# Kernel tuning notes

Measured on AMD Instinct MI355X. Metric: run time of the kernel, lower is better.

## Reference

```python
import jax, jax.numpy as jnp
import numpy as np

LEAKY_ALPHA = 0.2
EPS_NORM = 1e-07


def _leaky_relu(x):
    return jnp.where(x >= 0, x, LEAKY_ALPHA * x)


def setup_inputs() -> dict:
    key = jax.random.key(0)
    ks = jax.random.split(key, 10)
    B, N, F = 16, 1024, 256
    H, Q, K, V = 4, 128, 128, 128
    return {
        "e": jax.random.normal(ks[0], (B, N, N), dtype=jnp.float32),
        "x_atm": jax.random.normal(ks[1], (B, N, F), dtype=jnp.float32),
        "mask": jnp.ones((B, N), dtype=jnp.float32),
        "eps": jax.random.normal(ks[2], (1,), dtype=jnp.float32) * 0.02,
        "Wq": jax.random.normal(ks[3], (H, F, Q), dtype=jnp.float32) * 0.05,
        "Wk": jax.random.normal(ks[4], (H, F, K), dtype=jnp.float32) * 0.05,
        "Wv": jax.random.normal(ks[5], (H, F, V), dtype=jnp.float32) * 0.05,
        "aq": jax.random.normal(ks[6], (H, Q), dtype=jnp.float32) * 0.05,
        "bq": jnp.zeros((H,), dtype=jnp.float32),
        "ak": jax.random.normal(ks[7], (H, K), dtype=jnp.float32) * 0.05,
        "bk": jnp.zeros((H,), dtype=jnp.float32),
    }


def reference(e, x_atm, mask, eps, Wq, Wk, Wv, aq, bq, ak, bk):
    B, N, _ = e.shape
    # add learned eps to the diagonal of e (set_diag(diag + eps))
    e_mod = e + eps[0] * jnp.eye(N, dtype=e.dtype)  # [B,N,N]

    # per-head query/key scalars: Dense -> LeakyReLU -> Dense(1)
    q = jnp.einsum("bhnq,hq->bhn", _leaky_relu(jnp.einsum("bnf,hfq->bhnq", x_atm, Wq)), aq) + bq[None, :, None]  # [B,H,N]
    k = jnp.einsum("bhnk,hk->bhn", _leaky_relu(jnp.einsum("bnf,hfk->bhnk", x_atm, Wk)), ak) + bk[None, :, None]  # [B,H,N]

    # attn[b,h,i,j] = tanh((q_i + k_j) * e_mod[b,i,j])
    scores = jnp.tanh((q[..., :, None] + k[..., None, :]) * e_mod[:, None, :, :])  # [B,H,N,N]

    # L2-normalize each row (tf.linalg.normalize norm + 1e-7)
    norm = jnp.sqrt(jnp.sum(scores * scores, axis=-1, keepdims=True)) + EPS_NORM
    attn = scores / norm

    # values and aggregation
    v = jnp.einsum("bnf,hfv->bhnv", x_atm, Wv)  # [B,H,N,V] (dropout rate 0 -> identity)
    out = jnp.einsum("bhij,bhjv->bhiv", attn, v)  # [B,H,N,V]

    # pooling == 'mask': sum over nodes weighted by mask -> [B,H,V]
    pooled = jnp.einsum("bhnv,bn->bhv", out, mask)

    # concat heads along feature axis -> [B, H*V]
    return pooled.reshape(B, -1)
```

## Files before the change

### kernel.cpp

```cpp
#include <hip/hip_runtime.h>

#define B_ 16
#define N_ 1024
#define F_ 256
#define H_ 4
#define QDIM 128

#define TANH_PRESCALE 2.8853900817779268f

typedef __attribute__((ext_vector_type(8))) short bf16x8;
typedef __attribute__((ext_vector_type(4))) float f32x4;
typedef __attribute__((ext_vector_type(2))) float f32x2;

__device__ __forceinline__ float leaky(float x) {
    return x >= 0.f ? x : 0.2f * x;
}

__device__ __forceinline__ unsigned short bfbits(float f) {
    unsigned u = __float_as_uint(f);
    return (unsigned short)((u + 0x7fffu + ((u >> 16) & 1u)) >> 16);
}

__device__ __forceinline__ float bf2f(unsigned short u) {
    return __uint_as_float(((unsigned)u) << 16);
}

template <int CTRL>
__device__ __forceinline__ float dpp_add(float x) {
    return x + __int_as_float(
        __builtin_amdgcn_update_dpp(0, __float_as_int(x), CTRL, 0xf, 0xf, true));
}

__device__ __forceinline__ float wave_reduce_add(float x) {
    x = dpp_add<0xB1>(x);
    x = dpp_add<0x4E>(x);
    x = dpp_add<0x141>(x);
    x = dpp_add<0x140>(x);
    x += __shfl_xor(x, 16, 64);
    x += __shfl_xor(x, 32, 64);
    return x;
}

__global__ __launch_bounds__(256) void convert_all(
    const float4* __restrict__ x4, ushort4* __restrict__ xh4,
    const float* __restrict__ Wq, const float* __restrict__ Wk,
    ushort* __restrict__ Wqt, ushort* __restrict__ Wkt)
{
    const int bx = blockIdx.x;
    if (bx < 2048) {
        const int t = bx * 256 + threadIdx.x;
        const float4 a = x4[2 * t], b = x4[2 * t + 1];
        ushort4 o0, o1;
        o0.x = bfbits(a.x); o0.y = bfbits(a.y); o0.z = bfbits(a.z); o0.w = bfbits(a.w);
        o1.x = bfbits(b.x); o1.y = bfbits(b.y); o1.z = bfbits(b.z); o1.w = bfbits(b.w);
        xh4[2 * t] = o0; xh4[2 * t + 1] = o1;
    } else {
        const int t2 = (bx - 2048) * 256 + threadIdx.x;
        const int z = t2 >> 17, t = t2 & 131071;
        const int f = t & 255, q = (t >> 8) & 127, h = t >> 15;
        const float* W = z ? Wk : Wq;
        ushort* O = z ? Wkt : Wqt;
        O[t] = bfbits(W[(h * 256 + f) * 128 + q]);
    }
}

__global__ __launch_bounds__(256) void qk_mfma(
    const ushort* __restrict__ xh,
    const ushort* __restrict__ Wqt, const ushort* __restrict__ Wkt,
    const float* __restrict__ aq, const float* __restrict__ bq,
    const float* __restrict__ ak, const float* __restrict__ bk,
    float* __restrict__ qbuf, float* __restrict__ kbuf)
{
    const int tid = threadIdx.x;
    const int mt  = blockIdx.x;
    const int h   = blockIdx.y;
    const bool isQ = (blockIdx.z == 0);
    const ushort* Wt = isQ ? Wqt : Wkt;
    const float*  av = isQ ? aq : ak;
    const float*  bv = isQ ? bq : bk;
    float* out = isQ ? qbuf : kbuf;

    __shared__ char  xs[64 * 512];
    __shared__ float sp[4][64];

    {
        const int r = tid >> 2;
        const uint4* src = reinterpret_cast<const uint4*>(xh + (size_t)(mt * 64 + r) * 256);
        #pragma unroll
        for (int i = 0; i < 8; ++i) {
            const int c = (tid & 3) + 4 * i;
            const uint4 v = src[c];
            *reinterpret_cast<uint4*>(xs + r * 512 + ((c ^ (r & 7)) << 4)) = v;
        }
    }
    __syncthreads();

    const int l  = tid & 63, w = tid >> 6;
    const int g  = l >> 4, li = l & 15;

    bf16x8 Bf[8][2];
    #pragma unroll
    for (int nf = 0; nf < 2; ++nf) {
        const int c = w * 32 + nf * 16 + li;
        const ushort* bp = Wt + ((size_t)(h * 128 + c)) * 256 + 8 * g;
        #pragma unroll
        for (int s = 0; s < 8; ++s)
            Bf[s][nf] = *reinterpret_cast<const bf16x8*>(bp + s * 32);
    }

    f32x4 acc[4][2];
    #pragma unroll
    for (int m = 0; m < 4; ++m)
        #pragma unroll
        for (int nf = 0; nf < 2; ++nf)
            acc[m][nf] = (f32x4){0.f, 0.f, 0.f, 0.f};

    #pragma unroll
    for (int s = 0; s < 8; ++s) {
        #pragma unroll
        for (int m = 0; m < 4; ++m) {
            const int r = m * 16 + li;
            const int chunk = (4 * s + g) ^ (r & 7);
            const bf16x8 af = *reinterpret_cast<const bf16x8*>(xs + r * 512 + chunk * 16);
            acc[m][0] = __builtin_amdgcn_mfma_f32_16x16x32_bf16(af, Bf[s][0], acc[m][0], 0, 0, 0);
            acc[m][1] = __builtin_amdgcn_mfma_f32_16x16x32_bf16(af, Bf[s][1], acc[m][1], 0, 0, 0);
        }
    }

    float part[4][4];
    #pragma unroll
    for (int m = 0; m < 4; ++m)
        #pragma unroll
        for (int j = 0; j < 4; ++j) part[m][j] = 0.f;

    #pragma unroll
    for (int nf = 0; nf < 2; ++nf) {
        const float a_ = av[h * QDIM + w * 32 + nf * 16 + li];
        #pragma unroll
        for (int m = 0; m < 4; ++m)
            #pragma unroll
            for (int j = 0; j < 4; ++j)
                part[m][j] = fmaf(a_, leaky(acc[m][nf][j]), part[m][j]);
    }
    #pragma unroll
    for (int mask = 1; mask < 16; mask <<= 1)
        #pragma unroll
        for (int m = 0; m < 4; ++m)
            #pragma unroll
            for (int j = 0; j < 4; ++j)
                part[m][j] += __shfl_xor(part[m][j], mask, 64);

    if (li == 0) {
        #pragma unroll
        for (int m = 0; m < 4; ++m)
            #pragma unroll
            for (int j = 0; j < 4; ++j)
                sp[w][m * 16 + g * 4 + j] = part[m][j];
    }
    __syncthreads();

    if (tid < 64) {
        const float val = (sp[0][tid] + sp[1][tid] + sp[2][tid] + sp[3][tid] + bv[h]) * TANH_PRESCALE;
        const int R = mt * 64 + tid;
        out[((R >> 10) * H_ + h) * N_ + (R & 1023)] = val;
    }
}

__global__ __launch_bounds__(512) void attn_kernel(
    const float* __restrict__ e,
    const float* __restrict__ qbuf, const float* __restrict__ kbuf,
    const float* __restrict__ mask, const float* __restrict__ epsp,
    ushort* __restrict__ pbuf)
{
    const int tid  = threadIdx.x;
    const int wav  = tid >> 6;
    const int h    = wav & 3;
    const int half = wav >> 2;
    const int lane = tid & 63;
    const int b    = blockIdx.y;
    const int ic   = blockIdx.x;
    const int i0   = ic * 16 + half * 8;
    const float epsv = epsp[0];
    const int udiag = ic >> 4;

    __shared__ f32x2 red2[4][8][64];

    const f32x4* kr4 = reinterpret_cast<const f32x4*>(kbuf + (b * H_ + h) * N_);
    f32x2 kk2[8];
    #pragma unroll
    for (int u = 0; u < 4; ++u) {
        const f32x4 kv = kr4[u * 64 + lane];
        kk2[2 * u]     = __builtin_shufflevector(kv, kv, 0, 1);
        kk2[2 * u + 1] = __builtin_shufflevector(kv, kv, 2, 3);
    }

    f32x2 wacc2[8];
    #pragma unroll
    for (int p = 0; p < 8; ++p) wacc2[p] = (f32x2){0.f, 0.f};

    const float* qrow  = qbuf + (b * H_ + h) * N_;
    const float* mrow  = mask + b * N_;
    const f32x4* ebase = reinterpret_cast<const f32x4*>(e + ((size_t)b << 20)) + lane;

    const f32x2 one2 = {1.f, 1.f};
    const f32x2 m2   = {-2.f, -2.f};

    #pragma unroll
    for (int ii = 0; ii < 8; ii += 2) {
        const int iA = i0 + ii, iB = iA + 1;
        const float qiA = qrow[iA], qiB = qrow[iB];
        const f32x2 qiA2 = {qiA, qiA}, qiB2 = {qiB, qiB};
        const bool isdl = (lane == ((iA >> 2) & 63));
        const float daddA = isdl ? epsv : 0.f;
        const float daddB = daddA;

        const f32x4* erA = ebase + ((size_t)iA << 8);
        const f32x4* erB = ebase + ((size_t)iB << 8);
        f32x4 evA[4], evB[4];
        #pragma unroll
        for (int u = 0; u < 4; ++u) { evA[u] = erA[u * 64]; evB[u] = erB[u * 64]; }

        f32x2 pvA[8], pvB[8];
        f32x2 sslA = {0.f, 0.f}, sslB = {0.f, 0.f};
        #pragma unroll
        for (int u = 0; u < 4; ++u) {
            #pragma unroll
            for (int s = 0; s < 2; ++s) {
                const int p = 2 * u + s;
                const f32x2 eA2 = s ? __builtin_shufflevector(evA[u], evA[u], 2, 3)
                                    : __builtin_shufflevector(evA[u], evA[u], 0, 1);
                const f32x2 eB2 = s ? __builtin_shufflevector(evB[u], evB[u], 2, 3)
                                    : __builtin_shufflevector(evB[u], evB[u], 0, 1);
                const f32x2 qkA = qiA2 + kk2[p];
                const f32x2 qkB = qiB2 + kk2[p];
                f32x2 argA = qkA * eA2;
                f32x2 argB = qkB * eB2;
                if (u == udiag && s == ((ii & 3) >> 1)) {
                    argA[0] = fmaf(qkA[0], daddA, argA[0]);
                    argB[1] = fmaf(qkB[1], daddB, argB[1]);
                }
                f32x2 exA, exB;
                exA[0] = __builtin_amdgcn_exp2f(argA[0]);
                exB[0] = __builtin_amdgcn_exp2f(argB[0]);
                exA[1] = __builtin_amdgcn_exp2f(argA[1]);
                exB[1] = __builtin_amdgcn_exp2f(argB[1]);
                const f32x2 dA = exA + one2;
                const f32x2 dB = exB + one2;
                f32x2 rA, rB;
                rA[0] = __builtin_amdgcn_rcpf(dA[0]);
                rB[0] = __builtin_amdgcn_rcpf(dB[0]);
                rA[1] = __builtin_amdgcn_rcpf(dA[1]);
                rB[1] = __builtin_amdgcn_rcpf(dB[1]);
                const f32x2 pA = __builtin_elementwise_fma(rA, m2, one2);
                const f32x2 pB = __builtin_elementwise_fma(rB, m2, one2);
                pvA[p] = pA; pvB[p] = pB;
                sslA = __builtin_elementwise_fma(pA, pA, sslA);
                sslB = __builtin_elementwise_fma(pB, pB, sslB);
            }
        }
        const float sA = wave_reduce_add(sslA[0] + sslA[1]);
        const float sB = wave_reduce_add(sslB[0] + sslB[1]);
        const float scaleA = mrow[iA] * __builtin_amdgcn_rcpf(sqrtf(sA) + 1e-7f);
        const float scaleB = mrow[iB] * __builtin_amdgcn_rcpf(sqrtf(sB) + 1e-7f);
        const f32x2 scA = {scaleA, scaleA}, scB = {scaleB, scaleB};
        #pragma unroll
        for (int p = 0; p < 8; ++p) {
            wacc2[p] = __builtin_elementwise_fma(scA, pvA[p], wacc2[p]);
            wacc2[p] = __builtin_elementwise_fma(scB, pvB[p], wacc2[p]);
        }
    }

    if (half == 1) {
        #pragma unroll
        for (int p = 0; p < 8; ++p) red2[h][p][lane] = wacc2[p];
    }
    __syncthreads();
    if (half == 0) {
        ushort* pr = pbuf + ((size_t)((ic * 16 + b) * H_ + h) << 10);
        #pragma unroll
        for (int u = 0; u < 4; ++u) {
            const f32x2 a = wacc2[2 * u]     + red2[h][2 * u][lane];
            const f32x2 c = wacc2[2 * u + 1] + red2[h][2 * u + 1][lane];
            ushort4 o;
            o.x = bfbits(a[0]); o.y = bfbits(a[1]);
            o.z = bfbits(c[0]); o.w = bfbits(c[1]);
            *reinterpret_cast<ushort4*>(pr + u * 256 + lane * 4) = o;
        }
    }
}

__global__ __launch_bounds__(256) void ypart_kernel(
    const ushort* __restrict__ xh, const ushort* __restrict__ pbuf,
    float* __restrict__ ypart)
{
    const int tid = threadIdx.x;
    const int bx  = blockIdx.x;
    const int b   = bx >> 4;
    const int jc  = bx & 15;
    const int j0  = jc * 64;

    __shared__ float ws_[H_][64];
    {
        const int hh = tid >> 6, j = tid & 63;
        const ushort* pp = pbuf + ((size_t)(b * H_ + hh) << 10) + j0 + j;
        float s0 = 0.f, s1 = 0.f, s2 = 0.f, s3 = 0.f;
        #pragma unroll 4
        for (int ic = 0; ic < 64; ic += 4) {
            s0 += bf2f(pp[(size_t)(ic + 0) * 65536]);
            s1 += bf2f(pp[(size_t)(ic + 1) * 65536]);
            s2 += bf2f(pp[(size_t)(ic + 2) * 65536]);
            s3 += bf2f(pp[(size_t)(ic + 3) * 65536]);
        }
        ws_[hh][j] = (s0 + s1) + (s2 + s3);
    }
    __syncthreads();

    float a0 = 0.f, a1 = 0.f, a2 = 0.f, a3 = 0.f;
    const ushort* xcol = xh + ((size_t)(b * N_ + j0)) * F_ + tid;
    #pragma unroll 4
    for (int j = 0; j < 64; ++j) {
        const float xv = bf2f(xcol[(size_t)j * F_]);
        a0 = fmaf(ws_[0][j], xv, a0);
        a1 = fmaf(ws_[1][j], xv, a1);
        a2 = fmaf(ws_[2][j], xv, a2);
        a3 = fmaf(ws_[3][j], xv, a3);
    }
    float* yp = ypart + (size_t)(b * 16 + jc) * (H_ * F_) + tid;
    yp[0 * F_] = a0; yp[1 * F_] = a1; yp[2 * F_] = a2; yp[3 * F_] = a3;
}

__global__ __launch_bounds__(256) void pool_kernel(
    const float* __restrict__ ypart, const float* __restrict__ Wv,
    float* __restrict__ out)
{
    const int tid = threadIdx.x;
    const int bh  = blockIdx.x;
    const int b   = bh >> 2;
    const int h   = bh & 3;
    __shared__ float ys[256];
    float s = 0.f;
    #pragma unroll
    for (int jc = 0; jc < 16; ++jc)
        s += ypart[(size_t)(b * 16 + jc) * (H_ * F_) + h * F_ + tid];
    ys[tid] = s;
    __syncthreads();
    if (tid < 128) {
        float acc = 0.f;
        const float* wv = Wv + h * (F_ * 128) + tid;
        #pragma unroll 4
        for (int f = 0; f < F_; ++f) acc = fmaf(ys[f], wv[f * 128], acc);
        out[bh * 128 + tid] = acc;
    }
}

extern "C" void kernel_launch(void* const* d_in, const int* in_sizes, int n_in,
                              void* d_out, int out_size, void* d_ws, size_t ws_size,
                              hipStream_t stream) {
    const float* e    = (const float*)d_in[0];
    const float* x    = (const float*)d_in[1];
    const float* mask = (const float*)d_in[2];
    const float* eps  = (const float*)d_in[3];
    const float* Wq   = (const float*)d_in[4];
    const float* Wk   = (const float*)d_in[5];
    const float* Wv   = (const float*)d_in[6];
    const float* aq   = (const float*)d_in[7];
    const float* bq   = (const float*)d_in[8];
    const float* ak   = (const float*)d_in[9];
    const float* bk   = (const float*)d_in[10];

    float*  qbuf  = (float*)d_ws;
    float*  kbuf  = qbuf + 65536;
    float*  ypartb= kbuf + 65536;
    ushort* pbuf  = (ushort*)(ypartb + 262144);
    ushort* xh    = pbuf + 4194304;
    ushort* Wqt   = xh + 4194304;
    ushort* Wkt   = Wqt + 131072;
    float*  outf  = (float*)d_out;

    convert_all<<<3072, 256, 0, stream>>>((const float4*)x, (ushort4*)xh, Wq, Wk, Wqt, Wkt);
    qk_mfma<<<dim3(256, 4, 2), 256, 0, stream>>>(xh, Wqt, Wkt, aq, bq, ak, bk, qbuf, kbuf);
    attn_kernel<<<dim3(64, 16), 512, 0, stream>>>(e, qbuf, kbuf, mask, eps, pbuf);
    ypart_kernel<<<256, 256, 0, stream>>>(xh, pbuf, ypartb);
    pool_kernel<<<64, 256, 0, stream>>>(ypartb, Wv, outf);
}
```

Before: 80.20 us.

## Process two heads per wave sharing e rows instead of two rows per head

Each wave now handles two heads for 4 rows, so every loaded e row is reused across two heads rather than each wave loading two e rows for a single head. This halves per-wave e loads and redundant e traffic across the 4 head-waves, at the cost of an extra two-level shared-memory reduction across four row-quarter waves and more registers for two k vectors and accumulators.

```diff
diff --git a/kernel.cpp b/kernel.cpp
--- a/kernel.cpp
+++ b/kernel.cpp
@@ -174,51 +174,56 @@
 {
     const int tid  = threadIdx.x;
     const int wav  = tid >> 6;
-    const int h    = wav & 3;
-    const int half = wav >> 2;
+    const int qtr  = wav & 3;
+    const int hg   = wav >> 2;
+    const int hA   = hg * 2, hB = hg * 2 + 1;
     const int lane = tid & 63;
     const int b    = blockIdx.y;
     const int ic   = blockIdx.x;
-    const int i0   = ic * 16 + half * 8;
+    const int i0   = ic * 16 + qtr * 4;
     const float epsv = epsp[0];
     const int udiag = ic >> 4;
 
-    __shared__ f32x2 red2[4][8][64];
-
-    const f32x4* kr4 = reinterpret_cast<const f32x4*>(kbuf + (b * H_ + h) * N_);
-    f32x2 kk2[8];
+    __shared__ f32x2 red[2][2][2][8][64];
+
+    const f32x4* krA = reinterpret_cast<const f32x4*>(kbuf + (b * H_ + hA) * N_);
+    const f32x4* krB = reinterpret_cast<const f32x4*>(kbuf + (b * H_ + hB) * N_);
+    f32x2 kkA[8], kkB[8];
     #pragma unroll
     for (int u = 0; u < 4; ++u) {
-        const f32x4 kv = kr4[u * 64 + lane];
-        kk2[2 * u]     = __builtin_shufflevector(kv, kv, 0, 1);
-        kk2[2 * u + 1] = __builtin_shufflevector(kv, kv, 2, 3);
-    }
-
-    f32x2 wacc2[8];
-    #pragma unroll
-    for (int p = 0; p < 8; ++p) wacc2[p] = (f32x2){0.f, 0.f};
-
-    const float* qrow  = qbuf + (b * H_ + h) * N_;
+        const f32x4 ka = krA[u * 64 + lane];
+        const f32x4 kb = krB[u * 64 + lane];
+        kkA[2 * u]     = __builtin_shufflevector(ka, ka, 0, 1);
+        kkA[2 * u + 1] = __builtin_shufflevector(ka, ka, 2, 3);
+        kkB[2 * u]     = __builtin_shufflevector(kb, kb, 0, 1);
+        kkB[2 * u + 1] = __builtin_shufflevector(kb, kb, 2, 3);
+    }
+
+    f32x2 waccA[8], waccB[8];
+    #pragma unroll
+    for (int p = 0; p < 8; ++p) { waccA[p] = (f32x2){0.f, 0.f}; waccB[p] = (f32x2){0.f, 0.f}; }
+
+    const float* qrowA = qbuf + (b * H_ + hA) * N_;
+    const float* qrowB = qbuf + (b * H_ + hB) * N_;
     const float* mrow  = mask + b * N_;
     const f32x4* ebase = reinterpret_cast<const f32x4*>(e + ((size_t)b << 20)) + lane;
 
     const f32x2 one2 = {1.f, 1.f};
     const f32x2 m2   = {-2.f, -2.f};
 
-    #pragma unroll
-    for (int ii = 0; ii < 8; ii += 2) {
-        const int iA = i0 + ii, iB = iA + 1;
-        const float qiA = qrow[iA], qiB = qrow[iB];
+    const bool isdl = (lane == ((i0 >> 2) & 63));
+    const float dadd = isdl ? epsv : 0.f;
+
+    #pragma unroll
+    for (int ii = 0; ii < 4; ++ii) {
+        const int i = i0 + ii;
+        const float qiA = qrowA[i], qiB = qrowB[i];
         const f32x2 qiA2 = {qiA, qiA}, qiB2 = {qiB, qiB};
-        const bool isdl = (lane == ((iA >> 2) & 63));
-        const float daddA = isdl ? epsv : 0.f;
-        const float daddB = daddA;
-
-        const f32x4* erA = ebase + ((size_t)iA << 8);
-        const f32x4* erB = ebase + ((size_t)iB << 8);
-        f32x4 evA[4], evB[4];
-        #pragma unroll
-        for (int u = 0; u < 4; ++u) { evA[u] = erA[u * 64]; evB[u] = erB[u * 64]; }
+
+        const f32x4* er = ebase + ((size_t)i << 8);
+        f32x4 ev[4];
+        #pragma unroll
+        for (int u = 0; u < 4; ++u) ev[u] = er[u * 64];
 
         f32x2 pvA[8], pvB[8];
         f32x2 sslA = {0.f, 0.f}, sslB = {0.f, 0.f};
@@ -227,17 +232,16 @@
             #pragma unroll
             for (int s = 0; s < 2; ++s) {
                 const int p = 2 * u + s;
-                const f32x2 eA2 = s ? __builtin_shufflevector(evA[u], evA[u], 2, 3)
-                                    : __builtin_shufflevector(evA[u], evA[u], 0, 1);
-                const f32x2 eB2 = s ? __builtin_shufflevector(evB[u], evB[u], 2, 3)
-                                    : __builtin_shufflevector(evB[u], evB[u], 0, 1);
-                const f32x2 qkA = qiA2 + kk2[p];
-                const f32x2 qkB = qiB2 + kk2[p];
-                f32x2 argA = qkA * eA2;
-                f32x2 argB = qkB * eB2;
-                if (u == udiag && s == ((ii & 3) >> 1)) {
-                    argA[0] = fmaf(qkA[0], daddA, argA[0]);
-                    argB[1] = fmaf(qkB[1], daddB, argB[1]);
+                const f32x2 e2 = s ? __builtin_shufflevector(ev[u], ev[u], 2, 3)
+                                   : __builtin_shufflevector(ev[u], ev[u], 0, 1);
+                const f32x2 qkA = qiA2 + kkA[p];
+                const f32x2 qkB = qiB2 + kkB[p];
+                f32x2 argA = qkA * e2;
+                f32x2 argB = qkB * e2;
+                if (u == udiag && s == (ii >> 1)) {
+                    const int cc = ii & 1;
+                    argA[cc] = fmaf(qkA[cc], dadd, argA[cc]);
+                    argB[cc] = fmaf(qkB[cc], dadd, argB[cc]);
                 }
                 f32x2 exA, exB;
                 exA[0] = __builtin_amdgcn_exp2f(argA[0]);
@@ -260,31 +264,58 @@
         }
         const float sA = wave_reduce_add(sslA[0] + sslA[1]);
         const float sB = wave_reduce_add(sslB[0] + sslB[1]);
-        const float scaleA = mrow[iA] * __builtin_amdgcn_rcpf(sqrtf(sA) + 1e-7f);
-        const float scaleB = mrow[iB] * __builtin_amdgcn_rcpf(sqrtf(sB) + 1e-7f);
+        const float mi = mrow[i];
+        const float scaleA = mi * __builtin_amdgcn_rcpf(sqrtf(sA) + 1e-7f);
+        const float scaleB = mi * __builtin_amdgcn_rcpf(sqrtf(sB) + 1e-7f);
         const f32x2 scA = {scaleA, scaleA}, scB = {scaleB, scaleB};
         #pragma unroll
         for (int p = 0; p < 8; ++p) {
-            wacc2[p] = __builtin_elementwise_fma(scA, pvA[p], wacc2[p]);
-            wacc2[p] = __builtin_elementwise_fma(scB, pvB[p], wacc2[p]);
-        }
-    }
-
-    if (half == 1) {
-        #pragma unroll
-        for (int p = 0; p < 8; ++p) red2[h][p][lane] = wacc2[p];
-    }
-    __syncthreads();
-    if (half == 0) {
-        ushort* pr = pbuf + ((size_t)((ic * 16 + b) * H_ + h) << 10);
-        #pragma unroll
-        for (int u = 0; u < 4; ++u) {
-            const f32x2 a = wacc2[2 * u]     + red2[h][2 * u][lane];
-            const f32x2 c = wacc2[2 * u + 1] + red2[h][2 * u + 1][lane];
-            ushort4 o;
-            o.x = bfbits(a[0]); o.y = bfbits(a[1]);
-            o.z = bfbits(c[0]); o.w = bfbits(c[1]);
-            *reinterpret_cast<ushort4*>(pr + u * 256 + lane * 4) = o;
+            waccA[p] = __builtin_elementwise_fma(scA, pvA[p], waccA[p]);
+            waccB[p] = __builtin_elementwise_fma(scB, pvB[p], waccB[p]);
+        }
+    }
+
+    if (qtr & 1) {
+        #pragma unroll
+        for (int p = 0; p < 8; ++p) {
+            red[qtr >> 1][hg][0][p][lane] = waccA[p];
+            red[qtr >> 1][hg][1][p][lane] = waccB[p];
+        }
+    }
+    __syncthreads();
+    if (!(qtr & 1)) {
+        #pragma unroll
+        for (int p = 0; p < 8; ++p) {
+            waccA[p] += red[qtr >> 1][hg][0][p][lane];
+            waccB[p] += red[qtr >> 1][hg][1][p][lane];
+        }
+        if (qtr == 2) {
+            #pragma unroll
+            for (int p = 0; p < 8; ++p) {
+                red[1][hg][0][p][lane] = waccA[p];
+                red[1][hg][1][p][lane] = waccB[p];
+            }
+        }
+    }
+    __syncthreads();
+    if (qtr == 0) {
+        #pragma unroll
+        for (int p = 0; p < 8; ++p) {
+            waccA[p] += red[1][hg][0][p][lane];
+            waccB[p] += red[1][hg][1][p][lane];
+        }
+        #pragma unroll
+        for (int hh = 0; hh < 2; ++hh) {
+            ushort* pr = pbuf + ((size_t)((ic * 16 + b) * H_ + hA + hh) << 10);
+            #pragma unroll
+            for (int u = 0; u < 4; ++u) {
+                const f32x2 a = hh ? waccB[2 * u]     : waccA[2 * u];
+                const f32x2 c = hh ? waccB[2 * u + 1] : waccA[2 * u + 1];
+                ushort4 o;
+                o.x = bfbits(a[0]); o.y = bfbits(a[1]);
+                o.z = bfbits(c[0]); o.w = bfbits(c[1]);
+                *reinterpret_cast<ushort4*>(pr + u * 256 + lane * 4) = o;
+            }
         }
     }
 }
```

Result: slower. 86.93 us (+8.4%).
